# Performance work log

Hardware: AMD Instinct MI355X
Metric: run time of the kernel (lower is better)

Reference implementation:

```python
import jax, jax.numpy as jnp
import numpy as np

N, E, F_IN, F_OUT = 8192, 1024, 256, 256


def setup_inputs() -> dict:
    key = jax.random.key(0)
    k1, k2, k3, k4 = jax.random.split(key, 4)
    X = jax.random.normal(k1, (N, F_IN), dtype=jnp.float32)
    # binary incidence matrix: node i belongs to hyperedge j with p=0.05
    H = (jax.random.uniform(k2, (N, E)) < 0.05).astype(jnp.float32)
    W = jax.random.normal(k3, (F_OUT, F_IN), dtype=jnp.float32) * (1.0 / np.sqrt(F_IN))
    b = jax.random.normal(k4, (F_OUT,), dtype=jnp.float32) * 0.01
    return {"X": X, "H": H, "W": W, "b": b}


def reference(X, H, W, b):
    # Dv = diag(row sums of H), De = diag(col sums of H)
    dv = jnp.sum(H, axis=1)                      # [N] node degrees
    de = jnp.sum(H, axis=0)                      # [E] edge degrees
    dv_inv_sqrt = 1.0 / jnp.sqrt(dv)             # inv of sqrt(Dv) (diagonal)
    de_inv = 1.0 / de                            # inv of De (diagonal)
    # diagonal matrices realized as broadcast scalings (same math, no N x N).
    Xs = X * dv_inv_sqrt[:, None]
    M = H.T @ Xs                                 # H^T (...)          [E, F]
    M = M * de_inv[:, None]                      # De^-1 (...)        [E, F]
    X_new = (H @ M) * dv_inv_sqrt[:, None]       # Dv^-1/2 H (...)    [N, F]
    return X_new @ W.T + b                       # nn.Linear
```

## Files before the change

kernel.cpp:

```cpp
#include <hip/hip_runtime.h>
#include <hip/hip_bf16.h>
#include <stdint.h>

typedef __attribute__((ext_vector_type(8))) short bf16x8;
typedef __attribute__((ext_vector_type(4))) float f32x4;
typedef __attribute__((ext_vector_type(4))) unsigned int u32x4;
typedef __attribute__((ext_vector_type(2))) unsigned int u32x2;
typedef unsigned short u16;
typedef unsigned int u32;
typedef unsigned long long u64;

#define N_NODES 8192
#define N_EDGES 1024
#define F_DIM   256
#define NMAX 128

__device__ __forceinline__ u16 f2bf(float f) {
    union { float f; u32 u; } v; v.f = f;
    u32 u = v.u;
    u = (u + 0x7FFFu + ((u >> 16) & 1u)) >> 16;
    return (u16)u;
}
__device__ __forceinline__ float bflo(u32 p) {
    union { u32 u; float f; } v; v.u = p << 16; return v.f;
}
__device__ __forceinline__ float bfhi(u32 p) {
    union { u32 u; float f; } v; v.u = p & 0xffff0000u; return v.f;
}

__device__ __forceinline__ bf16x8 expand8(u32 byte) {
    union { u32 u[4]; bf16x8 v; } r;
#pragma unroll
    for (int i = 0; i < 4; ++i)
        r.u[i] = (((byte >> (2 * i)) & 1u) ? 0x3F80u : 0u)
               | (((byte >> (2 * i + 1)) & 1u) ? 0x3F800000u : 0u);
    return r.v;
}

__global__ __launch_bounds__(512) void prep(
    const float* __restrict__ H, const float* __restrict__ X,
    const float* __restrict__ W,
    float* __restrict__ dv, u16* __restrict__ nlist,
    u16* __restrict__ Xst, u32* __restrict__ HbTs, u16* __restrict__ Wb) {
    __shared__ u16 hmask[32][64];
    __shared__ u16 tT[256][34];
    const int tid = threadIdx.x;
    const int wv = tid >> 6;
    const int lane = tid & 63;
    const int blk = blockIdx.x;
    const int n0 = blk * 32 + wv * 4;

    f32x4 hv[4][4], xv[4];
#pragma unroll
    for (int r = 0; r < 4; ++r) {
        const int n = n0 + r;
#pragma unroll
        for (int q = 0; q < 4; ++q)
            hv[r][q] = *(const f32x4*)(&H[(size_t)n * N_EDGES + q * 256 + lane * 4]);
        xv[r] = *(const f32x4*)(&X[(size_t)n * F_DIM + lane * 4]);
    }

    if (wv == 7) {
        const f32x4 w = *(const f32x4*)(&W[(size_t)blk * F_DIM + lane * 4]);
        u32x2 pk;
        pk[0] = (u32)f2bf(w[0]) | ((u32)f2bf(w[1]) << 16);
        pk[1] = (u32)f2bf(w[2]) | ((u32)f2bf(w[3]) << 16);
        *(u32x2*)(&Wb[(size_t)blk * F_DIM + lane * 4]) = pk;
    }

#pragma unroll
    for (int r = 0; r < 4; ++r) {
        const int n = n0 + r;
        u32 m16 = 0u;
#pragma unroll
        for (int q = 0; q < 4; ++q)
#pragma unroll
            for (int j = 0; j < 4; ++j)
                m16 |= ((hv[r][q][j] != 0.f) ? 1u : 0u) << (q * 4 + j);
        hmask[wv * 4 + r][lane] = (u16)m16;
        const u32 cl = (u32)__popc(m16);
        u32 x = cl;
#pragma unroll
        for (int d = 1; d < 64; d <<= 1) {
            const u32 t = __shfl_up(x, d, 64);
            if (lane >= d) x += t;
        }
        const u32 total = __shfl(x, 63, 64);
        u32 pos = x - cl;
        u16* nrow = &nlist[(size_t)n * NMAX];
        u32 m = m16;
        while (m) {
            const int bidx = __builtin_ctz(m);
            m &= m - 1;
            const int col = ((bidx >> 2) << 8) + lane * 4 + (bidx & 3);
            if (pos < NMAX) nrow[pos] = (u16)col;
            ++pos;
        }
        if (lane == 0) dv[n] = (float)total;
        const float s = rsqrtf((float)total);
#pragma unroll
        for (int j = 0; j < 4; ++j)
            tT[lane * 4 + j][wv * 4 + r] = f2bf(xv[r][j] * s);
    }
    __syncthreads();
    {
        u32x2 st;
#pragma unroll
        for (int eo = 0; eo < 2; ++eo) {
            const int e = tid * 2 + eo;
            const int widx = (e & 255) >> 2;
            const int bit = ((e >> 8) << 2) + (e & 3);
            u32 w = 0u;
#pragma unroll
            for (int r = 0; r < 32; ++r)
                w |= (u32)((hmask[r][widx] >> bit) & 1u) << r;
            st[eo] = w;
        }
        *(u32x2*)(&HbTs[(size_t)blk * N_EDGES + tid * 2]) = st;
    }
    {
        const int f = tid & 255, half = tid >> 8;
        const u32* src = (const u32*)(&tT[f][half * 16]);
        u32x4 a, b2;
#pragma unroll
        for (int i = 0; i < 4; ++i) { a[i] = src[i]; b2[i] = src[i + 4]; }
        u16* dst = &Xst[(size_t)f * N_NODES + blk * 32 + half * 16];
        *(u32x4*)dst = a;
        *(u32x4*)(dst + 8) = b2;
    }
}

__global__ __launch_bounds__(256) void gemm1(
    const u16* __restrict__ Xst, const u32* __restrict__ HbTs,
    u16* __restrict__ Mb) {
    __shared__ float red[4][2][64][4];
    __shared__ float cnts[4][2][16];
    const int tid = threadIdx.x;
    const int wv = tid >> 6, lane = tid & 63;
    const int e0 = (blockIdx.x & 31) * 32;
    const int f0 = (blockIdx.x >> 5) * 16;
    const int row16 = lane & 15, quad = lane >> 4;
    const int C0 = wv * 32;
    const u16* bp = Xst + (size_t)(f0 + row16) * N_NODES + quad * 8;
    const u32* wp = HbTs + e0 + row16;

    f32x4 acc[2] = {};
    u32 cnt0 = 0, cnt1 = 0;

    auto LOAD = [&](u32x4 (&B)[4][2], u32 (&Wd)[4][2][2], int base) {
#pragma unroll
        for (int c = 0; c < 4; ++c) {
            const size_t k0 = (size_t)(C0 + base + c) * 64;
#pragma unroll
            for (int ks = 0; ks < 2; ++ks)
                B[c][ks] = *(const u32x4*)(bp + k0 + ks * 32);
            const size_t s0 = (size_t)(C0 + base + c) * 2 * N_EDGES;
#pragma unroll
            for (int ks = 0; ks < 2; ++ks)
#pragma unroll
                for (int eh = 0; eh < 2; ++eh)
                    Wd[c][ks][eh] = wp[s0 + (size_t)ks * N_EDGES + eh * 16];
        }
    };
    auto COMP = [&](u32x4 (&B)[4][2], u32 (&Wd)[4][2][2]) {
#pragma unroll
        for (int c = 0; c < 4; ++c)
#pragma unroll
            for (int ks = 0; ks < 2; ++ks) {
                union { u32x4 u; bf16x8 v; } bu; bu.u = B[c][ks];
                const u32 b0 = (Wd[c][ks][0] >> (quad * 8)) & 0xFFu;
                const u32 b1 = (Wd[c][ks][1] >> (quad * 8)) & 0xFFu;
                cnt0 += (u32)__popc(b0); cnt1 += (u32)__popc(b1);
                acc[0] = __builtin_amdgcn_mfma_f32_16x16x32_bf16(expand8(b0), bu.v, acc[0], 0, 0, 0);
                acc[1] = __builtin_amdgcn_mfma_f32_16x16x32_bf16(expand8(b1), bu.v, acc[1], 0, 0, 0);
            }
    };

    u32x4 Ba[4][2], Bb[4][2];
    u32   Wa[4][2][2], Wc[4][2][2];
    LOAD(Ba, Wa, 0);
    for (int b = 0; b < 32; b += 8) {
        LOAD(Bb, Wc, b + 4);
        COMP(Ba, Wa);
        LOAD(Ba, Wa, min(b + 8, 28));
        COMP(Bb, Wc);
    }

    cnt0 += __shfl_down(cnt0, 32, 64); cnt0 += __shfl_down(cnt0, 16, 64);
    cnt1 += __shfl_down(cnt1, 32, 64); cnt1 += __shfl_down(cnt1, 16, 64);
    if (lane < 16) {
        cnts[wv][0][lane] = (float)cnt0;
        cnts[wv][1][lane] = (float)cnt1;
    }
#pragma unroll
    for (int eh = 0; eh < 2; ++eh)
        *(f32x4*)(&red[wv][eh][lane][0]) = acc[eh];
    __syncthreads();
    if (wv < 2) {
        const int eh = wv;
        f32x4 s = {};
#pragma unroll
        for (int w = 0; w < 4; ++w) {
            const f32x4 v = *(const f32x4*)(&red[w][eh][lane][0]);
            s[0] += v[0]; s[1] += v[1]; s[2] += v[2]; s[3] += v[3];
        }
#pragma unroll
        for (int r = 0; r < 4; ++r) {
            const int ei = quad * 4 + r;
            const float de = cnts[0][eh][ei] + cnts[1][eh][ei] +
                             cnts[2][eh][ei] + cnts[3][eh][ei];
            const int el = eh * 16 + ei;
            Mb[(size_t)(e0 + el) * F_DIM + f0 + row16] = f2bf(s[r] / de);
        }
    }
}

__global__ __launch_bounds__(512) void spmm2w(
    const u16* __restrict__ Mb, const float* __restrict__ dv,
    const u16* __restrict__ nlist, const u16* __restrict__ Wb,
    const float* __restrict__ bias, float* __restrict__ out) {
    __shared__ u16 nl[8 * NMAX];
    __shared__ u16 Yb[8][264];
    const int tid = threadIdx.x;
    const int wv = tid >> 6;
    const int lane = tid & 63;
    const int n0 = blockIdx.x * 8;
    ((u32*)nl)[tid] = ((const u32*)&nlist[(size_t)n0 * NMAX])[tid];
    __syncthreads();
    const int half = lane >> 5, l32 = lane & 31;
    const int n = n0 + wv;
    const float dvn = dv[n];
    const int cnt = min((int)dvn, NMAX);
    const u16* lt = &nl[wv * NMAX];
    float a[8] = {};
    const int npairs = (cnt + 1) >> 1;
#pragma unroll 8
    for (int p = 0; p < npairs; ++p) {
        const int idx0 = 2 * p + half;
        const int idx = min(idx0, cnt - 1);
        const float msk = (idx0 < cnt) ? 1.f : 0.f;
        const int e = lt[idx];
        const u32x4 pk = *(const u32x4*)(&Mb[(size_t)e * F_DIM + l32 * 8]);
        a[0] = fmaf(bflo(pk[0]), msk, a[0]); a[1] = fmaf(bfhi(pk[0]), msk, a[1]);
        a[2] = fmaf(bflo(pk[1]), msk, a[2]); a[3] = fmaf(bfhi(pk[1]), msk, a[3]);
        a[4] = fmaf(bflo(pk[2]), msk, a[4]); a[5] = fmaf(bfhi(pk[2]), msk, a[5]);
        a[6] = fmaf(bflo(pk[3]), msk, a[6]); a[7] = fmaf(bfhi(pk[3]), msk, a[7]);
    }
#pragma unroll
    for (int k = 0; k < 8; ++k) a[k] += __shfl_xor(a[k], 32, 64);
    const float s = rsqrtf(dvn);
    if (half == 0) {
        u32x4 pk;
        pk[0] = (u32)f2bf(a[0] * s) | ((u32)f2bf(a[1] * s) << 16);
        pk[1] = (u32)f2bf(a[2] * s) | ((u32)f2bf(a[3] * s) << 16);
        pk[2] = (u32)f2bf(a[4] * s) | ((u32)f2bf(a[5] * s) << 16);
        pk[3] = (u32)f2bf(a[6] * s) | ((u32)f2bf(a[7] * s) << 16);
        *(u32x4*)(&Yb[wv][l32 * 8]) = pk;
    }
    __syncthreads();
    const int row16 = lane & 15, quad = lane >> 4;
    f32x4 acc[2] = {};
    for (int ko = 0; ko < 256; ko += 32) {
        bf16x8 af = {};
        if (row16 < 8)
            af = *(const bf16x8*)(&Yb[row16][ko + quad * 8]);
#pragma unroll
        for (int tn = 0; tn < 2; ++tn) {
            const int j = wv * 32 + tn * 16 + row16;
            const bf16x8 bf = *(const bf16x8*)(&Wb[(size_t)j * F_DIM + ko + quad * 8]);
            acc[tn] = __builtin_amdgcn_mfma_f32_16x16x32_bf16(af, bf, acc[tn], 0, 0, 0);
        }
    }
#pragma unroll
    for (int tn = 0; tn < 2; ++tn) {
        const int col = wv * 32 + tn * 16 + row16;
        const float bc = bias[col];
#pragma unroll
        for (int r2 = 0; r2 < 4; ++r2) {
            const int row = quad * 4 + r2;
            if (row < 8)
                out[(size_t)(n0 + row) * F_DIM + col] = acc[tn][r2] + bc;
        }
    }
}

extern "C" void kernel_launch(void* const* d_in, const int* in_sizes, int n_in,
                              void* d_out, int out_size, void* d_ws, size_t ws_size,
                              hipStream_t stream) {
    (void)in_sizes; (void)n_in; (void)out_size; (void)ws_size;
    const float* X = (const float*)d_in[0];
    const float* H = (const float*)d_in[1];
    const float* W = (const float*)d_in[2];
    const float* b = (const float*)d_in[3];
    float* out = (float*)d_out;

    char* ws = (char*)d_ws;
    float* dv    = (float*)(ws);
    u32*   HbTs  = (u32*)(ws + 0x10000);
    u16*   nlist = (u16*)(ws + 0x110000);
    u16*   Xst   = (u16*)(ws + 0x310000);
    u16*   Mb    = (u16*)(ws + 0x710000);
    u16*   Wb    = (u16*)(ws + 0x790000);

    prep<<<256, 512, 0, stream>>>(H, X, W, dv, nlist, Xst, HbTs, Wb);
    gemm1<<<512, 256, 0, stream>>>(Xst, HbTs, Mb);
    spmm2w<<<N_NODES / 8, 512, 0, stream>>>(Mb, dv, nlist, Wb, b, out);
}
```

Before: 142.5 us.

## Restructure gemm1 with async global-to-LDS double buffering and larger tiles

Rewrites the H^T·X gemm kernel so that 8 waves each own a K-slice and stream X tiles into LDS via global_load_lds async copies, double-buffered, with hand-placed waitcnt. The block tile grows to 32 edges by 32 features so each A fragment (expanded from the incidence bits) is reused across two B tiles. The grid halves to 256 blocks of 512 threads. The cross-wave reduction moves to a padded LDS buffer with all threads writing outputs. This trades register-direct loads for LDS staging and uses 64KB of shared memory, which lowers occupancy and adds a fixed vmcnt assumption that must match the number of outstanding loads.

```diff
diff --git a/kernel.cpp b/kernel.cpp
--- a/kernel.cpp
+++ b/kernel.cpp
@@ -8,6 +8,7 @@
 typedef __attribute__((ext_vector_type(2))) unsigned int u32x2;
 typedef unsigned short u16;
 typedef unsigned int u32;
+typedef unsigned char u8;
 typedef unsigned long long u64;
 
 #define N_NODES 8192
@@ -26,6 +27,12 @@
 }
 __device__ __forceinline__ float bfhi(u32 p) {
     union { u32 u; float f; } v; v.u = p & 0xffff0000u; return v.f;
+}
+
+__device__ __forceinline__ void async16(const u16* g, u16* l) {
+    __builtin_amdgcn_global_load_lds(
+        (const __attribute__((address_space(1))) u32*)(const void*)g,
+        (__attribute__((address_space(3))) u32*)(void*)l, 16, 0, 0);
 }
 
 __device__ __forceinline__ bf16x8 expand8(u32 byte) {
@@ -130,60 +137,74 @@
     }
 }
 
-__global__ __launch_bounds__(256) void gemm1(
+__global__ __launch_bounds__(512) void gemm1(
     const u16* __restrict__ Xst, const u32* __restrict__ HbTs,
     u16* __restrict__ Mb) {
-    __shared__ float red[4][2][64][4];
-    __shared__ float cnts[4][2][16];
+    __shared__ __align__(16) u8 smem[65536];
+    __shared__ float cnts[8][2][16];
     const int tid = threadIdx.x;
     const int wv = tid >> 6, lane = tid & 63;
-    const int e0 = (blockIdx.x & 31) * 32;
-    const int f0 = (blockIdx.x >> 5) * 16;
+    const int f0 = ((int)blockIdx.x & 7) * 32;
+    const int e0 = ((int)blockIdx.x >> 3) * 32;
     const int row16 = lane & 15, quad = lane >> 4;
-    const int C0 = wv * 32;
-    const u16* bp = Xst + (size_t)(f0 + row16) * N_NODES + quad * 8;
-    const u32* wp = HbTs + e0 + row16;
-
-    f32x4 acc[2] = {};
+    const int srow = lane & 15, schunk = lane >> 4;
+    u16* myBs = (u16*)(smem + wv * 8192);
+    const int kbase = wv * 1024;
+
+    f32x4 acc[2][2] = {};
     u32 cnt0 = 0, cnt1 = 0;
-
-    auto LOAD = [&](u32x4 (&B)[4][2], u32 (&Wd)[4][2][2], int base) {
-#pragma unroll
-        for (int c = 0; c < 4; ++c) {
-            const size_t k0 = (size_t)(C0 + base + c) * 64;
+    u32 wA[2][2], wB[2][2];
+
+    auto STAGE = [&](int it, int buf) {
+        __builtin_amdgcn_sched_barrier(0);
+        const int k0 = kbase + it * 64;
+#pragma unroll
+        for (int tn = 0; tn < 2; ++tn)
 #pragma unroll
             for (int ks = 0; ks < 2; ++ks)
-                B[c][ks] = *(const u32x4*)(bp + k0 + ks * 32);
-            const size_t s0 = (size_t)(C0 + base + c) * 2 * N_EDGES;
+                async16(Xst + (size_t)(f0 + tn * 16 + srow) * N_NODES + k0 + ks * 32 + schunk * 8,
+                        myBs + buf * 2048 + (tn * 2 + ks) * 512);
+    };
+    auto LOADW = [&](int it, u32 (&w)[2][2]) {
+        const int k0 = kbase + it * 64;
+#pragma unroll
+        for (int tm = 0; tm < 2; ++tm)
 #pragma unroll
             for (int ks = 0; ks < 2; ++ks)
-#pragma unroll
-                for (int eh = 0; eh < 2; ++eh)
-                    Wd[c][ks][eh] = wp[s0 + (size_t)ks * N_EDGES + eh * 16];
-        }
+                w[tm][ks] = HbTs[(size_t)((k0 >> 5) + ks) * N_EDGES + e0 + tm * 16 + row16];
     };
-    auto COMP = [&](u32x4 (&B)[4][2], u32 (&Wd)[4][2][2]) {
-#pragma unroll
-        for (int c = 0; c < 4; ++c)
-#pragma unroll
-            for (int ks = 0; ks < 2; ++ks) {
-                union { u32x4 u; bf16x8 v; } bu; bu.u = B[c][ks];
-                const u32 b0 = (Wd[c][ks][0] >> (quad * 8)) & 0xFFu;
-                const u32 b1 = (Wd[c][ks][1] >> (quad * 8)) & 0xFFu;
-                cnt0 += (u32)__popc(b0); cnt1 += (u32)__popc(b1);
-                acc[0] = __builtin_amdgcn_mfma_f32_16x16x32_bf16(expand8(b0), bu.v, acc[0], 0, 0, 0);
-                acc[1] = __builtin_amdgcn_mfma_f32_16x16x32_bf16(expand8(b1), bu.v, acc[1], 0, 0, 0);
+    auto COMPUTE = [&](int buf, u32 (&w)[2][2]) {
+        asm volatile("s_waitcnt vmcnt(4)" ::: "memory");
+        __builtin_amdgcn_sched_barrier(0);
+#pragma unroll
+        for (int ks = 0; ks < 2; ++ks) {
+            bf16x8 bfr[2];
+#pragma unroll
+            for (int tn = 0; tn < 2; ++tn)
+                bfr[tn] = *(const bf16x8*)(myBs + buf * 2048 + (tn * 2 + ks) * 512 + lane * 8);
+#pragma unroll
+            for (int tm = 0; tm < 2; ++tm) {
+                const u32 byte = (w[tm][ks] >> (quad * 8)) & 0xFFu;
+                if (tm == 0) cnt0 += (u32)__popc(byte); else cnt1 += (u32)__popc(byte);
+                const bf16x8 af = expand8(byte);
+#pragma unroll
+                for (int tn = 0; tn < 2; ++tn)
+                    acc[tm][tn] = __builtin_amdgcn_mfma_f32_16x16x32_bf16(
+                        af, bfr[tn], acc[tm][tn], 0, 0, 0);
             }
+        }
     };
 
-    u32x4 Ba[4][2], Bb[4][2];
-    u32   Wa[4][2][2], Wc[4][2][2];
-    LOAD(Ba, Wa, 0);
-    for (int b = 0; b < 32; b += 8) {
-        LOAD(Bb, Wc, b + 4);
-        COMP(Ba, Wa);
-        LOAD(Ba, Wa, min(b + 8, 28));
-        COMP(Bb, Wc);
+    STAGE(0, 0);
+    LOADW(0, wA);
+    for (int i = 0; i < 8; ++i) {
+        STAGE(2 * i + 1, 1);
+        LOADW(2 * i + 1, wB);
+        COMPUTE(0, wA);
+        const int nxt = (2 * i + 2 < 16) ? (2 * i + 2) : 15;
+        STAGE(nxt, 0);
+        LOADW(nxt, wA);
+        COMPUTE(1, wB);
     }
 
     cnt0 += __shfl_down(cnt0, 32, 64); cnt0 += __shfl_down(cnt0, 16, 64);
@@ -192,25 +213,36 @@
         cnts[wv][0][lane] = (float)cnt0;
         cnts[wv][1][lane] = (float)cnt1;
     }
-#pragma unroll
-    for (int eh = 0; eh < 2; ++eh)
-        *(f32x4*)(&red[wv][eh][lane][0]) = acc[eh];
-    __syncthreads();
-    if (wv < 2) {
-        const int eh = wv;
-        f32x4 s = {};
-#pragma unroll
-        for (int w = 0; w < 4; ++w) {
-            const f32x4 v = *(const f32x4*)(&red[w][eh][lane][0]);
-            s[0] += v[0]; s[1] += v[1]; s[2] += v[2]; s[3] += v[3];
-        }
-#pragma unroll
-        for (int r = 0; r < 4; ++r) {
-            const int ei = quad * 4 + r;
-            const float de = cnts[0][eh][ei] + cnts[1][eh][ei] +
-                             cnts[2][eh][ei] + cnts[3][eh][ei];
-            const int el = eh * 16 + ei;
-            Mb[(size_t)(e0 + el) * F_DIM + f0 + row16] = f2bf(s[r] / de);
+    __syncthreads();
+    {
+        float* redf = (float*)smem;
+        float* my = &redf[(size_t)(wv * 64 + lane) * 17];
+#pragma unroll
+        for (int tm = 0; tm < 2; ++tm)
+#pragma unroll
+            for (int tn = 0; tn < 2; ++tn)
+#pragma unroll
+                for (int r = 0; r < 4; ++r)
+                    my[tm * 8 + tn * 4 + r] = acc[tm][tn][r];
+    }
+    __syncthreads();
+    {
+        const float* redf = (const float*)smem;
+#pragma unroll
+        for (int h = 0; h < 2; ++h) {
+            const int idx = tid + h * 512;
+            const int el = idx >> 5, fl = idx & 31;
+            const int tm = el >> 4, q = (el >> 2) & 3, r = el & 3;
+            const int tn = fl >> 4, r16 = fl & 15;
+            const int srcl = q * 16 + r16;
+            const int j = tm * 8 + tn * 4 + r;
+            float s = 0.f, de = 0.f;
+#pragma unroll
+            for (int w = 0; w < 8; ++w) {
+                s += redf[(size_t)(w * 64 + srcl) * 17 + j];
+                de += cnts[w][tm][el & 15];
+            }
+            Mb[(size_t)(e0 + el) * F_DIM + f0 + fl] = f2bf(s / de);
         }
     }
 }
@@ -303,6 +335,6 @@
     u16*   Wb    = (u16*)(ws + 0x790000);
 
     prep<<<256, 512, 0, stream>>>(H, X, W, dv, nlist, Xst, HbTs, Wb);
-    gemm1<<<512, 256, 0, stream>>>(Xst, HbTs, Mb);
+    gemm1<<<256, 512, 0, stream>>>(Xst, HbTs, Mb);
     spmm2w<<<N_NODES / 8, 512, 0, stream>>>(Mb, dv, nlist, Wb, b, out);
 }
```

Result: faster. 138.4 us (-2.9%).
